# Performance work log

Hardware: AMD Instinct MI355X
Metric: run time of the kernel (lower is better)

## Reference

```python
import jax, jax.numpy as jnp
import numpy as np
from jax import lax

T, K, D = 2097152, 8, 4
LOG_2PI = float(np.log(2.0 * np.pi))


def setup_inputs() -> dict:
    key = jax.random.key(0)
    k1, k2, k3, k4 = jax.random.split(key, 4)
    return {
        "x_seq": jax.random.normal(k1, (T, D), dtype=jnp.float32),
        "unnormalized_trans": jax.random.normal(k2, (K, K), dtype=jnp.float32),
        "unnormalized_pi": jax.random.normal(k3, (K,), dtype=jnp.float32),
        "means": jax.random.normal(k4, (K, D), dtype=jnp.float32) * 0.01,
        "log_std": jnp.zeros((K, D), dtype=jnp.float32),
    }


def reference(x_seq, unnormalized_trans, unnormalized_pi, means, log_std):
    # Row-stochastic transition / initial distributions in log space
    log_trans = jax.nn.log_softmax(unnormalized_trans, axis=-1)  # [K, K]
    log_pi = jax.nn.log_softmax(unnormalized_pi, axis=-1)        # [K]

    # Diagonal-Gaussian log emission densities: [T, K]
    std = jnp.exp(log_std)                                        # [K, D]
    z = (x_seq[:, None, :] - means[None, :, :]) / std[None, :, :]  # [T, K, D]
    log_em = jnp.sum(-0.5 * LOG_2PI - log_std[None] - 0.5 * z * z, axis=-1)  # [T, K]

    # Forward algorithm in log space (strictly sequential recurrence)
    alpha0 = log_pi + log_em[0]  # [K]

    def step(alpha, em_t):
        # alpha[i] + log_trans[i, j], logsumexp over source state i
        alpha = em_t + jax.scipy.special.logsumexp(alpha[:, None] + log_trans, axis=0)
        return alpha, None

    alpha, _ = lax.scan(step, alpha0, log_em[1:])
    return jax.scipy.special.logsumexp(alpha, axis=0)
```

## Files before the change

kernel.cpp:

```cpp
#include <hip/hip_runtime.h>
#include <math.h>

#define T_LEN 2097152
#define K 8
#define D 4
#define CHUNK 8
#define TPB 256
#define NBLK (T_LEN / (CHUNK * TPB))
#define MS4 19

typedef float f2 __attribute__((ext_vector_type(2)));

__device__ __forceinline__ f2 fma2(f2 a, f2 b, f2 c) { return __builtin_elementwise_fma(a, b, c); }
__device__ __forceinline__ f2 max2(f2 a, f2 b) { return __builtin_elementwise_max(a, b); }
__device__ __forceinline__ f2 splat(float s) { f2 r; r.x = s; r.y = s; return r; }


__device__ __forceinline__ float4* matp4(float* lm, int li) {
    return reinterpret_cast<float4*>(lm) + li * MS4 + ((li >> 1) & 3);
}

__device__ __forceinline__ void renorm2(f2 M[K][4], float& shift) {
    f2 m2 = max2(max2(M[0][0], M[0][1]), max2(M[0][2], M[0][3]));
#pragma unroll
    for (int i = 1; i < K; ++i)
        m2 = max2(m2, max2(max2(M[i][0], M[i][1]), max2(M[i][2], M[i][3])));
    float mx = fmaxf(m2.x, m2.y);
    int ex = (__float_as_int(mx) >> 23) & 255;
    float scale = __int_as_float((254 - ex) << 23);
    shift += (float)(ex - 127);
    f2 sc = splat(scale);
#pragma unroll
    for (int i = 0; i < K; ++i)
#pragma unroll
        for (int jj = 0; jj < 4; ++jj) M[i][jj] = M[i][jj] * sc;
}

__device__ __forceinline__ void store_mat(float* lm, int li, const f2 M[K][4]) {
    float4* dst = matp4(lm, li);
#pragma unroll
    for (int i = 0; i < K; ++i) {
        float4 w0, w1;
        w0.x = M[i][0].x; w0.y = M[i][0].y; w0.z = M[i][1].x; w0.w = M[i][1].y;
        w1.x = M[i][2].x; w1.y = M[i][2].y; w1.z = M[i][3].x; w1.w = M[i][3].y;
        dst[i * 2] = w0;
        dst[i * 2 + 1] = w1;
    }
}

__device__ __forceinline__ void combine8(float* lm, float* lsh, int li, int ri, int i) {
    const float4* Lb = matp4(lm, li);
    const float4* Rb = matp4(lm, ri);
    float4 la = Lb[i * 2], lb = Lb[i * 2 + 1];
    float4 R[16];
#pragma unroll
    for (int q = 0; q < 16; ++q) R[q] = Rb[q];
    float lk[8] = {la.x, la.y, la.z, la.w, lb.x, lb.y, lb.z, lb.w};
    f2 acc[4];
#pragma unroll
    for (int k = 0; k < 8; ++k) {
        f2 s = splat(lk[k]);
        f2 r0, r1, r2_, r3;
        r0.x = R[2 * k].x;     r0.y = R[2 * k].y;
        r1.x = R[2 * k].z;     r1.y = R[2 * k].w;
        r2_.x = R[2 * k + 1].x; r2_.y = R[2 * k + 1].y;
        r3.x = R[2 * k + 1].z;  r3.y = R[2 * k + 1].w;
        if (k == 0) {
            acc[0] = s * r0; acc[1] = s * r1; acc[2] = s * r2_; acc[3] = s * r3;
        } else {
            acc[0] = fma2(s, r0, acc[0]); acc[1] = fma2(s, r1, acc[1]);
            acc[2] = fma2(s, r2_, acc[2]); acc[3] = fma2(s, r3, acc[3]);
        }
    }
    f2 m2 = max2(max2(acc[0], acc[1]), max2(acc[2], acc[3]));
    float mx = fmaxf(m2.x, m2.y);
    mx = fmaxf(mx, __shfl_xor(mx, 1));
    mx = fmaxf(mx, __shfl_xor(mx, 2));
    mx = fmaxf(mx, __shfl_xor(mx, 4));
    int ex = (__float_as_int(mx) >> 23) & 255;
    float scale = __int_as_float((254 - ex) << 23);
    float ns = lsh[li] + lsh[ri] + (float)(ex - 127);
    f2 sc = splat(scale);
    f2 o0 = acc[0] * sc, o1 = acc[1] * sc, o2 = acc[2] * sc, o3 = acc[3] * sc;
    float4 w0, w1;
    w0.x = o0.x; w0.y = o0.y; w0.z = o1.x; w0.w = o1.y;
    w1.x = o2.x; w1.y = o2.y; w1.z = o3.x; w1.w = o3.y;
    float4* Ob = matp4(lm, li);
    Ob[i * 2] = w0;
    Ob[i * 2 + 1] = w1;
    if (i == 0) lsh[li] = ns;
}

__device__ __forceinline__ void tree_levels(float* lm, float* lsh) {
    const int g = threadIdx.x >> 3;
    const int i = threadIdx.x & 7;
#pragma unroll 1
    for (int lvl = 1; lvl <= 3; ++lvl) {
        const int c = 64 >> (lvl - 1);
        const int S = 1 << (lvl - 1);
#pragma unroll 1
        for (int m = g; m < c; m += 32) combine8(lm, lsh, 2 * m * S, 2 * m * S + S, i);
        __syncthreads();
    }
    if (threadIdx.x < 64) {
#pragma unroll 1
        for (int lvl = 4; lvl <= 7; ++lvl) {
            const int c = 64 >> (lvl - 1);
            const int S = 1 << (lvl - 1);
            if (g < c) combine8(lm, lsh, 2 * g * S, 2 * g * S + S, i);
            asm volatile("s_waitcnt lgkmcnt(0)" ::: "memory");
        }
    }
}

__device__ __forceinline__ void hybrid_tree(f2 P2[K][4], float shift, float* lm, float* lsh) {
    const int t = threadIdx.x;
    if ((t & 1) == 0) {
        store_mat(lm, t >> 1, P2);
        lsh[t >> 1] = shift;
    }
    __syncthreads();
    if (t & 1) {
        const float4* src = matp4(lm, t >> 1);
        float lsv = lsh[t >> 1];
        f2 C[K][4];
#pragma unroll
        for (int i = 0; i < K; ++i) {
            float4 la = src[i * 2], lb = src[i * 2 + 1];
            float lk[8] = {la.x, la.y, la.z, la.w, lb.x, lb.y, lb.z, lb.w};
            f2 q[4];
#pragma unroll
            for (int k = 0; k < 8; ++k) {
                f2 s = splat(lk[k]);
                if (k == 0) {
#pragma unroll
                    for (int jj = 0; jj < 4; ++jj) q[jj] = s * P2[k][jj];
                } else {
#pragma unroll
                    for (int jj = 0; jj < 4; ++jj) q[jj] = fma2(s, P2[k][jj], q[jj]);
                }
            }
#pragma unroll
            for (int jj = 0; jj < 4; ++jj) C[i][jj] = q[jj];
        }
        float ns = shift + lsv;
        renorm2(C, ns);
        store_mat(lm, t >> 1, C);
        lsh[t >> 1] = ns;
    }
    __syncthreads();
    tree_levels(lm, lsh);
}

__device__ __forceinline__ float emit_e2(const f2 ca2[4], const f2 cb2[4][4],
                                         const f2 cc2[4][4], float4 x, f2 e2[4]) {
    f2 x0 = splat(x.x), x1 = splat(x.y), x2 = splat(x.z), x3 = splat(x.w);
    f2 em2[4];
#pragma unroll
    for (int jj = 0; jj < 4; ++jj) {
        f2 t = ca2[jj];
        t = fma2(fma2(cc2[0][jj], x0, cb2[0][jj]), x0, t);
        t = fma2(fma2(cc2[1][jj], x1, cb2[1][jj]), x1, t);
        t = fma2(fma2(cc2[2][jj], x2, cb2[2][jj]), x2, t);
        t = fma2(fma2(cc2[3][jj], x3, cb2[3][jj]), x3, t);
        em2[jj] = t;
    }
    f2 m2 = max2(max2(em2[0], em2[1]), max2(em2[2], em2[3]));
    float me = fmaxf(m2.x, m2.y);
#pragma unroll
    for (int jj = 0; jj < 4; ++jj) {
        e2[jj].x = exp2f(em2[jj].x - me);
        e2[jj].y = exp2f(em2[jj].y - me);
    }
    return me;
}

__global__ void hmm_setup(const float* __restrict__ x,
                          const float* __restrict__ ut,
                          const float* __restrict__ up,
                          const float* __restrict__ mn,
                          const float* __restrict__ lsd,
                          float* __restrict__ ws) {
    const int lane = threadIdx.x;
    const float L2PI = 1.83787706640934548356f;
    const float LOG2E = 1.44269504088896340736f;

    float v = ut[lane];
    float m = v;
    m = fmaxf(m, __shfl_xor(m, 1));
    m = fmaxf(m, __shfl_xor(m, 2));
    m = fmaxf(m, __shfl_xor(m, 4));
    float e = expf(v - m);
    float s = e;
    s += __shfl_xor(s, 1); s += __shfl_xor(s, 2); s += __shfl_xor(s, 4);
    ws[lane] = e / s;

    float pv = up[lane & 7];
    float pm = pv;
    pm = fmaxf(pm, __shfl_xor(pm, 1));
    pm = fmaxf(pm, __shfl_xor(pm, 2));
    pm = fmaxf(pm, __shfl_xor(pm, 4));
    float pe = expf(pv - pm);
    float ps = pe;
    ps += __shfl_xor(ps, 1); ps += __shfl_xor(ps, 2); ps += __shfl_xor(ps, 4);
    float pival = pe / ps;

    int k = (lane & 31) >> 2, d = lane & 3;
    float lv = lsd[k * D + d];
    float mu = mn[k * D + d];
    float iv = expf(-2.f * lv);
    float bn = mu * iv;
    float cn = -0.5f * iv;
    float aterm = -0.5f * L2PI - lv - 0.5f * mu * mu * iv;
    float ak = aterm;
    ak += __shfl_xor(ak, 1); ak += __shfl_xor(ak, 2);
    if (lane < 32) {
        ws[72 + lane]  = bn * LOG2E;
        ws[104 + lane] = cn * LOG2E;
        if (d == 0) ws[64 + k] = ak * LOG2E;
    }

    float xd = x[d];
    float part = (cn * xd + bn) * xd + aterm;
    part += __shfl_xor(part, 1); part += __shfl_xor(part, 2);
    float pik = __shfl(pival, k);
    if (lane < 32 && d == 0) ws[136 + k] = pik * expf(part);
}

__global__ __launch_bounds__(TPB) void hmm_main(const float* __restrict__ x,
                                                const float* __restrict__ cst,
                                                float* __restrict__ bp,
                                                float* __restrict__ bs) {
    __shared__ __align__(16) float lm[128 * 76];
    __shared__ float lsh[128];
    const int tid = blockIdx.x * TPB + threadIdx.x;

    float Tr[K][K];
#pragma unroll
    for (int i = 0; i < K; ++i)
#pragma unroll
        for (int j = 0; j < K; ++j) Tr[i][j] = cst[i * K + j];
    f2 Tr2[K][4];
#pragma unroll
    for (int i = 0; i < K; ++i)
#pragma unroll
        for (int jj = 0; jj < 4; ++jj) { Tr2[i][jj].x = Tr[i][2 * jj]; Tr2[i][jj].y = Tr[i][2 * jj + 1]; }

    f2 ca2[4], cb2[4][4], cc2[4][4];
#pragma unroll
    for (int jj = 0; jj < 4; ++jj) {
        ca2[jj].x = cst[64 + 2 * jj]; ca2[jj].y = cst[64 + 2 * jj + 1];
#pragma unroll
        for (int d = 0; d < 4; ++d) {
            cb2[d][jj].x = cst[72 + (2 * jj) * 4 + d];  cb2[d][jj].y = cst[72 + (2 * jj + 1) * 4 + d];
            cc2[d][jj].x = cst[104 + (2 * jj) * 4 + d]; cc2[d][jj].y = cst[104 + (2 * jj + 1) * 4 + d];
        }
    }

    const float4* xv = reinterpret_cast<const float4*>(x) + (size_t)tid * CHUNK;
    float4 xr[CHUNK];
#pragma unroll
    for (int t = 0; t < CHUNK; ++t) xr[t] = xv[t];

    f2 T2[K][4];
    float shift;
    {
        f2 eB[4];
        float meB = emit_e2(ca2, cb2, cc2, xr[1], eB);
        if (tid == 0) {
#pragma unroll
            for (int i = 0; i < K; ++i) {
                f2 a0 = splat(cst[136 + i]);
#pragma unroll
                for (int jj = 0; jj < 4; ++jj) T2[i][jj] = a0 * Tr2[i][jj] * eB[jj];
            }
            shift = meB;
        } else {
            f2 eA[4];
            float meA = emit_e2(ca2, cb2, cc2, xr[0], eA);
#pragma unroll
            for (int i = 0; i < K; ++i) {
                f2 ei = splat((i & 1) ? eA[i >> 1].y : eA[i >> 1].x);
#pragma unroll
                for (int jj = 0; jj < 4; ++jj) T2[i][jj] = ei * Tr2[i][jj] * eB[jj];
            }
            shift = meA + meB;
        }
    }

#pragma unroll
    for (int p = 1; p < 4; ++p) {
        f2 eA[4], eB[4];
        float meA = emit_e2(ca2, cb2, cc2, xr[2 * p], eA);
        float meB = emit_e2(ca2, cb2, cc2, xr[2 * p + 1], eB);
        shift += meA + meB;
#pragma unroll
        for (int i = 0; i < K; ++i) {
            f2 r2[4];
#pragma unroll
            for (int kk = 0; kk < 4; ++kk) r2[kk] = T2[i][kk] * eA[kk];
            f2 u[4];
#pragma unroll
            for (int jj = 0; jj < 4; ++jj) u[jj] = splat(r2[0].x) * Tr2[0][jj];
#pragma unroll
            for (int k = 1; k < 8; ++k) {
                f2 rk = splat((k & 1) ? r2[k >> 1].y : r2[k >> 1].x);
#pragma unroll
                for (int jj = 0; jj < 4; ++jj) u[jj] = fma2(rk, Tr2[k][jj], u[jj]);
            }
#pragma unroll
            for (int jj = 0; jj < 4; ++jj) T2[i][jj] = u[jj] * eB[jj];
        }
    }

    if (tid != 0) {
#pragma unroll
        for (int jj = 0; jj < 4; ++jj) {
            f2 c[K];
#pragma unroll
            for (int k = 0; k < K; ++k) c[k] = T2[k][jj];
#pragma unroll
            for (int i = 0; i < K; ++i) {
                f2 a = splat(Tr[i][0]) * c[0];
#pragma unroll
                for (int k = 1; k < K; ++k) a = fma2(splat(Tr[i][k]), c[k], a);
                T2[i][jj] = a;
            }
        }
    }

    renorm2(T2, shift);

    hybrid_tree(T2, shift, lm, lsh);

    if (threadIdx.x == 0) {
        float4* o4 = reinterpret_cast<float4*>(bp + (size_t)blockIdx.x * 64);
        const float4* l4 = reinterpret_cast<const float4*>(lm);
#pragma unroll
        for (int q = 0; q < 16; ++q) o4[q] = l4[q];
        bs[blockIdx.x] = lsh[0];
    }
}

__global__ __launch_bounds__(TPB) void hmm_final(const float* __restrict__ bp,
                                                 const float* __restrict__ bs,
                                                 float* __restrict__ out) {
    __shared__ __align__(16) float lm[128 * 76];
    __shared__ float lsh[128];
    const int t = threadIdx.x;
    const int base = t * 4;

    f2 P2[K][4];
    {
        const float4* p4 = reinterpret_cast<const float4*>(bp + (size_t)base * 64);
#pragma unroll
        for (int i = 0; i < K; ++i) {
            float4 a = p4[2 * i], b = p4[2 * i + 1];
            P2[i][0].x = a.x; P2[i][0].y = a.y;
            P2[i][1].x = a.z; P2[i][1].y = a.w;
            P2[i][2].x = b.x; P2[i][2].y = b.y;
            P2[i][3].x = b.z; P2[i][3].y = b.w;
        }
    }
    float shift = bs[base];
#pragma unroll 1
    for (int r = 1; r < 4; ++r) {
        const float4* r4 = reinterpret_cast<const float4*>(bp + (size_t)(base + r) * 64);
        float4 R[16];
#pragma unroll
        for (int q = 0; q < 16; ++q) R[q] = r4[q];
        f2 C[K][4];
#pragma unroll
        for (int i = 0; i < K; ++i) {
            f2 q[4];
#pragma unroll
            for (int k = 0; k < 8; ++k) {
                float pk_ = (k & 1) ? P2[i][k >> 1].y : P2[i][k >> 1].x;
                f2 s = splat(pk_);
                f2 r0, r1, r2_, r3;
                r0.x = R[2 * k].x;      r0.y = R[2 * k].y;
                r1.x = R[2 * k].z;      r1.y = R[2 * k].w;
                r2_.x = R[2 * k + 1].x; r2_.y = R[2 * k + 1].y;
                r3.x = R[2 * k + 1].z;  r3.y = R[2 * k + 1].w;
                if (k == 0) {
                    q[0] = s * r0; q[1] = s * r1; q[2] = s * r2_; q[3] = s * r3;
                } else {
                    q[0] = fma2(s, r0, q[0]); q[1] = fma2(s, r1, q[1]);
                    q[2] = fma2(s, r2_, q[2]); q[3] = fma2(s, r3, q[3]);
                }
            }
#pragma unroll
            for (int jj = 0; jj < 4; ++jj) C[i][jj] = q[jj];
        }
        shift += bs[base + r];
        renorm2(C, shift);
#pragma unroll
        for (int i = 0; i < K; ++i)
#pragma unroll
            for (int jj = 0; jj < 4; ++jj) P2[i][jj] = C[i][jj];
    }

    hybrid_tree(P2, shift, lm, lsh);

    if (t == 0) {
        double s = 0.0;
#pragma unroll
        for (int i = 0; i < 64; ++i) s += (double)lm[i];
        out[0] = (float)(log(s) + (double)lsh[0] * 0.69314718055994530942);
    }
}

extern "C" void kernel_launch(void* const* d_in, const int* in_sizes, int n_in,
                              void* d_out, int out_size, void* d_ws, size_t ws_size,
                              hipStream_t stream) {
    (void)in_sizes; (void)n_in; (void)out_size; (void)ws_size;
    const float* x  = (const float*)d_in[0];
    const float* ut = (const float*)d_in[1];
    const float* up = (const float*)d_in[2];
    const float* mn = (const float*)d_in[3];
    const float* ls = (const float*)d_in[4];
    float* ws  = (float*)d_ws;
    float* out = (float*)d_out;
    float* bp  = ws + 256;
    float* bs  = ws + 256 + (size_t)NBLK * 64;

    hmm_setup<<<1, 64, 0, stream>>>(x, ut, up, mn, ls, ws);
    hmm_main<<<NBLK, TPB, 0, stream>>>(x, ws, bp, bs);
    hmm_final<<<1, TPB, 0, stream>>>(bp, bs, out);
}
```

Baseline: 124.5 us.

## Split final block-matrix reduction into parallel mid stage plus tiny final kernel

The single-block final kernel, which serially multiplied four 8x8 block matrices per thread before a tree reduction, is replaced by two stages. An 8-block mid kernel tree-reduces 128 block products each in shared memory, and a 64-thread final kernel combines the 8 results. This spreads the tail reduction across more compute units but adds one more kernel launch and a global round-trip.

```diff
diff --git a/kernel.cpp b/kernel.cpp
--- a/kernel.cpp
+++ b/kernel.cpp
@@ -8,6 +8,7 @@
 #define TPB 256
 #define NBLK (T_LEN / (CHUNK * TPB))
 #define MS4 19
+#define NMID 8
 
 typedef float f2 __attribute__((ext_vector_type(2)));
 
@@ -342,70 +343,69 @@
     }
 }
 
-__global__ __launch_bounds__(TPB) void hmm_final(const float* __restrict__ bp,
-                                                 const float* __restrict__ bs,
-                                                 float* __restrict__ out) {
+__global__ __launch_bounds__(TPB) void hmm_mid(const float* __restrict__ bp,
+                                               const float* __restrict__ bs,
+                                               float* __restrict__ bp2,
+                                               float* __restrict__ bs2) {
     __shared__ __align__(16) float lm[128 * 76];
     __shared__ float lsh[128];
     const int t = threadIdx.x;
-    const int base = t * 4;
-
-    f2 P2[K][4];
+    const int m = t >> 1;
+    const int h = t & 1;
+    const int gbase = blockIdx.x * 128;
+
     {
-        const float4* p4 = reinterpret_cast<const float4*>(bp + (size_t)base * 64);
-#pragma unroll
-        for (int i = 0; i < K; ++i) {
-            float4 a = p4[2 * i], b = p4[2 * i + 1];
-            P2[i][0].x = a.x; P2[i][0].y = a.y;
-            P2[i][1].x = a.z; P2[i][1].y = a.w;
-            P2[i][2].x = b.x; P2[i][2].y = b.y;
-            P2[i][3].x = b.z; P2[i][3].y = b.w;
-        }
-    }
-    float shift = bs[base];
-#pragma unroll 1
-    for (int r = 1; r < 4; ++r) {
-        const float4* r4 = reinterpret_cast<const float4*>(bp + (size_t)(base + r) * 64);
-        float4 R[16];
-#pragma unroll
-        for (int q = 0; q < 16; ++q) R[q] = r4[q];
-        f2 C[K][4];
-#pragma unroll
-        for (int i = 0; i < K; ++i) {
-            f2 q[4];
-#pragma unroll
-            for (int k = 0; k < 8; ++k) {
-                float pk_ = (k & 1) ? P2[i][k >> 1].y : P2[i][k >> 1].x;
-                f2 s = splat(pk_);
-                f2 r0, r1, r2_, r3;
-                r0.x = R[2 * k].x;      r0.y = R[2 * k].y;
-                r1.x = R[2 * k].z;      r1.y = R[2 * k].w;
-                r2_.x = R[2 * k + 1].x; r2_.y = R[2 * k + 1].y;
-                r3.x = R[2 * k + 1].z;  r3.y = R[2 * k + 1].w;
-                if (k == 0) {
-                    q[0] = s * r0; q[1] = s * r1; q[2] = s * r2_; q[3] = s * r3;
-                } else {
-                    q[0] = fma2(s, r0, q[0]); q[1] = fma2(s, r1, q[1]);
-                    q[2] = fma2(s, r2_, q[2]); q[3] = fma2(s, r3, q[3]);
-                }
-            }
-#pragma unroll
-            for (int jj = 0; jj < 4; ++jj) C[i][jj] = q[jj];
-        }
-        shift += bs[base + r];
-        renorm2(C, shift);
-#pragma unroll
-        for (int i = 0; i < K; ++i)
-#pragma unroll
-            for (int jj = 0; jj < 4; ++jj) P2[i][jj] = C[i][jj];
-    }
-
-    hybrid_tree(P2, shift, lm, lsh);
+        const float4* src = reinterpret_cast<const float4*>(bp + (size_t)(gbase + m) * 64) + h * 8;
+        float4 v[8];
+#pragma unroll
+        for (int q = 0; q < 8; ++q) v[q] = src[q];
+        float4* dst = matp4(lm, m) + h * 8;
+#pragma unroll
+        for (int q = 0; q < 8; ++q) dst[q] = v[q];
+    }
+    if (t < 128) lsh[t] = bs[gbase + t];
+    __syncthreads();
+
+    tree_levels(lm, lsh);
+
+    if (t == 0) {
+        float4* o4 = reinterpret_cast<float4*>(bp2 + (size_t)blockIdx.x * 64);
+        const float4* l4 = reinterpret_cast<const float4*>(lm);
+#pragma unroll
+        for (int q = 0; q < 16; ++q) o4[q] = l4[q];
+        bs2[blockIdx.x] = lsh[0];
+    }
+}
+
+__global__ __launch_bounds__(64) void hmm_final(const float* __restrict__ bp2,
+                                                const float* __restrict__ bs2,
+                                                float* __restrict__ out) {
+    __shared__ __align__(16) float lm[8 * 76];
+    __shared__ float lsh[8];
+    const int t = threadIdx.x;
+    const int g = t >> 3;
+    const int i = t & 7;
+
+    {
+        const float4* src = reinterpret_cast<const float4*>(bp2 + (size_t)g * 64) + i * 2;
+        float4 a = src[0], b = src[1];
+        float4* dst = matp4(lm, g) + i * 2;
+        dst[0] = a; dst[1] = b;
+    }
+    if (i == 0) lsh[g] = bs2[g];
+    __syncthreads();
+
+    if (g < 4) combine8(lm, lsh, 2 * g, 2 * g + 1, i);
+    __syncthreads();
+    if (g < 2) combine8(lm, lsh, 4 * g, 4 * g + 2, i);
+    __syncthreads();
+    if (g < 1) combine8(lm, lsh, 0, 4, i);
+    __syncthreads();
 
     if (t == 0) {
         double s = 0.0;
 #pragma unroll
-        for (int i = 0; i < 64; ++i) s += (double)lm[i];
+        for (int q = 0; q < 64; ++q) s += (double)lm[q];
         out[0] = (float)(log(s) + (double)lsh[0] * 0.69314718055994530942);
     }
 }
@@ -422,9 +422,12 @@
     float* ws  = (float*)d_ws;
     float* out = (float*)d_out;
     float* bp  = ws + 256;
-    float* bs  = ws + 256 + (size_t)NBLK * 64;
+    float* bs  = bp + (size_t)NBLK * 64;
+    float* bp2 = bs + NBLK;
+    float* bs2 = bp2 + (size_t)NMID * 64;
 
     hmm_setup<<<1, 64, 0, stream>>>(x, ut, up, mn, ls, ws);
     hmm_main<<<NBLK, TPB, 0, stream>>>(x, ws, bp, bs);
-    hmm_final<<<1, TPB, 0, stream>>>(bp, bs, out);
-}
+    hmm_mid<<<NMID, TPB, 0, stream>>>(bp, bs, bp2, bs2);
+    hmm_final<<<1, 64, 0, stream>>>(bp2, bs2, out);
+}
```

After: 121.4 us. 2.5% less time.
